# Performance work log

Hardware: AMD Instinct MI355X
Metric: run time of the kernel (lower is better)

Reference implementation:

```python
import jax, jax.numpy as jnp
import numpy as np

B_SZ, L, D_IN, D_MODEL, N_LAYERS, D_STATE, D_OUT = 32, 1024, 128, 256, 4, 64, 10
N2 = D_STATE // 2  # complex conjugate-pair modes


def setup_inputs() -> dict:
    key = jax.random.key(0)
    ks = jax.random.split(key, 12)
    H, N = D_MODEL, N2
    x = jax.random.normal(ks[0], (B_SZ, L, D_IN), jnp.float32)
    enc_w = jax.random.normal(ks[1], (D_IN, H), jnp.float32) / np.float32(np.sqrt(D_IN))
    enc_b = jnp.zeros((H,), jnp.float32)
    # S4D-diag params (diag-lin measure, real_type=exp): A = -exp(A_re_log) + i*A_im
    log_dt = jax.random.uniform(ks[2], (N_LAYERS, H), jnp.float32,
                                minval=np.float32(np.log(1e-3)), maxval=np.float32(np.log(1e-1)))
    A_re_log = jnp.full((N_LAYERS, H, N), np.float32(np.log(0.5)), jnp.float32)
    A_im = jnp.broadcast_to(np.float32(np.pi) * jnp.arange(N, dtype=jnp.float32),
                            (N_LAYERS, H, N)).copy()
    B_re = jnp.ones((N_LAYERS, H, N), jnp.float32)
    B_im = jnp.zeros((N_LAYERS, H, N), jnp.float32)
    C_re = jax.random.normal(ks[3], (N_LAYERS, H, N), jnp.float32) * np.float32(0.5 ** 0.5)
    C_im = jax.random.normal(ks[4], (N_LAYERS, H, N), jnp.float32) * np.float32(0.5 ** 0.5)
    D = jax.random.normal(ks[5], (N_LAYERS, H), jnp.float32)
    ln_w = jnp.ones((N_LAYERS, H), jnp.float32)
    ln_b = jnp.zeros((N_LAYERS, H), jnp.float32)
    out_w = jax.random.normal(ks[6], (N_LAYERS, H, 2 * H), jnp.float32) / np.float32(np.sqrt(H))
    out_b = jnp.zeros((N_LAYERS, 2 * H), jnp.float32)
    dec_w = jax.random.normal(ks[7], (H, D_OUT), jnp.float32) / np.float32(np.sqrt(H))
    dec_b = jnp.zeros((D_OUT,), jnp.float32)
    return dict(x=x, enc_w=enc_w, enc_b=enc_b, log_dt=log_dt, A_re_log=A_re_log, A_im=A_im,
                B_re=B_re, B_im=B_im, C_re=C_re, C_im=C_im, D=D, ln_w=ln_w, ln_b=ln_b,
                out_w=out_w, out_b=out_b, dec_w=dec_w, dec_b=dec_b)


def _layernorm(x, w, b):
    m = x.mean(-1, keepdims=True)
    v = ((x - m) ** 2).mean(-1, keepdims=True)
    return (x - m) * jax.lax.rsqrt(v + 1e-5) * w + b


def _s4_block(u, log_dt, A_re_log, A_im, B_re, B_im, C_re, C_im, Dp, out_w, out_b):
    # u: (B, L, H). Diagonal S4 (S4D) with ZOH discretization, FFT long-conv.
    H, N = A_re_log.shape
    Lq = u.shape[1]
    A = -jnp.exp(A_re_log) + 1j * A_im            # (H, N) complex, Re<0 stable
    dt = jnp.exp(log_dt)[:, None]                 # (H, 1)
    Bc = B_re + 1j * B_im
    Cc = C_re + 1j * C_im
    dtA = dt * A                                  # (H, N)
    dA = jnp.exp(dtA)
    dB = Bc * (dA - 1.0) / A                      # ZOH input matrix
    # Vandermonde kernel: K[h, l] = 2 * Re( sum_n C*dB * exp(dtA)^l )
    ell = jnp.arange(Lq, dtype=jnp.float32)
    P = jnp.exp(dtA[:, :, None] * ell)            # (H, N, L)
    K = 2.0 * jnp.einsum('hn,hnl->hl', Cc * dB, P).real  # (H, L) float32
    # causal conv via FFT at length 2L
    n_fft = 2 * Lq
    Kf = jnp.fft.rfft(K, n=n_fft, axis=-1)        # (H, L+1)
    Uf = jnp.fft.rfft(u, n=n_fft, axis=1)         # (B, L+1, H)
    y = jnp.fft.irfft(Uf * Kf.T[None], n=n_fft, axis=1)[:, :Lq]  # (B, L, H)
    y = y + u * Dp                                # skip connection D*u
    y = jax.nn.gelu(y)
    z = y @ out_w + out_b                         # position-wise output linear
    return z[..., :H] * jax.nn.sigmoid(z[..., H:])  # GLU


def reference(x, enc_w, enc_b, log_dt, A_re_log, A_im, B_re, B_im, C_re, C_im, D,
              ln_w, ln_b, out_w, out_b, dec_w, dec_b):
    h = x @ enc_w + enc_b                         # encoder: (B, L, d_model)
    for i in range(N_LAYERS):                     # postnorm residual stack
        z = _s4_block(h, log_dt[i], A_re_log[i], A_im[i], B_re[i], B_im[i],
                      C_re[i], C_im[i], D[i], out_w[i], out_b[i])
        h = z + h
        h = _layernorm(h, ln_w[i], ln_b[i])
    return h @ dec_w + dec_b                      # decoder: (B, L, d_output)
```

## Files before the change

### kernel.cpp

```cpp
#include <hip/hip_runtime.h>
#include <hip/hip_bf16.h>
#include <math.h>

#define B_SZ    32
#define LSEQ    1024
#define DIN     128
#define HDIM    256
#define NLAYERS 4
#define NSTATE  32
#define DOUT    10
#define M_ROWS  (B_SZ*LSEQ)
#define CH      64
#define NCH     (LSEQ/CH)
#define NBC     (B_SZ*NCH)

typedef __hip_bfloat16 bf16;
typedef __attribute__((ext_vector_type(8))) short bf16x8;
typedef __attribute__((ext_vector_type(4))) float f32x4;

__device__ __forceinline__ unsigned short f2bu(float x) {
    bf16 b = __float2bfloat16(x);
    return *(unsigned short*)&b;
}
__device__ __forceinline__ float bu2f(unsigned short u) {
    bf16 b = *(bf16*)&u;
    return __bfloat162float(b);
}

__device__ __forceinline__ float4 s4param(const float* __restrict__ log_dt,
                                          const float* __restrict__ A_re_log,
                                          const float* __restrict__ A_im,
                                          const float* __restrict__ B_re,
                                          const float* __restrict__ B_im,
                                          const float* __restrict__ C_re,
                                          const float* __restrict__ C_im,
                                          int layer, int h, int n) {
    int hn = layer * HDIM + h;
    int idx = hn * NSTATE + n;
    float dt   = expf(log_dt[hn]);
    float Are  = -expf(A_re_log[idx]);
    float Aim  = A_im[idx];
    float dtAre = dt * Are, dtAim = dt * Aim;
    float ea   = expf(dtAre);
    float dAre = ea * cosf(dtAim), dAim = ea * sinf(dtAim);
    float nre = dAre - 1.0f, nim = dAim;
    float inv = 1.0f / (Are * Are + Aim * Aim);
    float tre = (nre * Are + nim * Aim) * inv;
    float tim = (nim * Are - nre * Aim) * inv;
    float Brv = B_re[idx], Biv = B_im[idx];
    float dBre = Brv * tre - Biv * tim;
    float dBim = Brv * tim + Biv * tre;
    float Crv = C_re[idx], Civ = C_im[idx];
    float Wre = Crv * dBre - Civ * dBim;
    float Wim = Crv * dBim + Civ * dBre;
    return make_float4(dtAre, dtAim, Wre, Wim);
}

#define VMB_ (NLAYERS*HDIM*64*32/256)
#define TDB_ ((NLAYERS*HDIM*66+255)/256)
#define PAB_ (NLAYERS*NSTATE*HDIM/256)
#define WCB_ (NLAYERS*512*256/256)
__global__ void k_setup(const float* __restrict__ log_dt, const float* __restrict__ A_re_log,
                        const float* __restrict__ A_im, const float* __restrict__ B_re,
                        const float* __restrict__ B_im, const float* __restrict__ C_re,
                        const float* __restrict__ C_im, const float* __restrict__ out_w,
                        const float* __restrict__ enc_w, float* __restrict__ Td,
                        bf16* __restrict__ Vg, bf16* __restrict__ Mg,
                        float2* __restrict__ PA64, bf16* __restrict__ Wt,
                        bf16* __restrict__ Wet) {
    const float inv2pi = 0.15915494309189535f;
    const float twopi  = 6.283185307179586f;
    int bx = blockIdx.x;
    if (bx < VMB_) {
        int gid = bx * 256 + threadIdx.x;
        int jp = (gid & 31) * 2;
        int row = gid >> 5;
        int comp = row & 63, h = (row >> 6) & 255, layer = row >> 14;
        int n = comp >> 1, isIm = comp & 1;
        float4 q = s4param(log_dt, A_re_log, A_im, B_re, B_im, C_re, C_im, layer, h, n);
        unsigned int vpk = 0, mpk = 0;
#pragma unroll
        for (int e = 0; e < 2; ++e) {
            int j = jp + e;
            float dv = (float)(63 - j);
            float magv = __expf(dv * q.x);
            float pr = dv * q.y * inv2pi;
            float th = (pr - floorf(pr)) * twopi;
            float c = __cosf(th), s = __sinf(th);
            float vre = magv * (q.z * c - q.w * s);
            float vim = magv * (q.z * s + q.w * c);
            vpk |= (unsigned int)f2bu(isIm ? vim : vre) << (16 * e);
            float dm = (float)(j + 1);
            float magm = __expf(dm * q.x);
            float pr2 = dm * q.y * inv2pi;
            float th2 = (pr2 - floorf(pr2)) * twopi;
            float mv = isIm ? (-2.f * magm * __sinf(th2)) : (2.f * magm * __cosf(th2));
            mpk |= (unsigned int)f2bu(mv) << (16 * e);
        }
        {
            int mtv = comp >> 4, frv = comp & 15;
            int ksv = jp >> 5, qdv = (jp >> 3) & 3, ev = jp & 7;
            size_t voff = (size_t)(layer * 256 + h) * 4096
                        + ((size_t)((mtv * 2 + ksv) * 64) + qdv * 16 + frv) * 8 + ev;
            ((unsigned int*)Vg)[voff >> 1] = vpk;
        }
        ((unsigned int*)Mg)[(size_t)row * 32 + (jp >> 1)] = mpk;
    } else if (bx < VMB_ + TDB_) {
        int gid = (bx - VMB_) * 256 + threadIdx.x;
        int d = gid % 66;
        int lh = gid / 66;
        if (lh < NLAYERS * HDIM && d < 65) {
            int layer = lh >> 8, h = lh & 255;
            float fd = (float)d;
            float acc = 0.f;
            for (int n = 0; n < NSTATE; ++n) {
                float4 q = s4param(log_dt, A_re_log, A_im, B_re, B_im, C_re, C_im, layer, h, n);
                float mag = __expf(fd * q.x);
                float pr = fd * q.y * inv2pi;
                float th = (pr - floorf(pr)) * twopi;
                acc += mag * (q.z * __cosf(th) - q.w * __sinf(th));
            }
            Td[(size_t)lh * 66 + d] = 2.f * acc;
        }
    } else if (bx < VMB_ + TDB_ + PAB_) {
        int idx = (bx - VMB_ - TDB_) * 256 + threadIdx.x;
        int h = idx & 255, n = (idx >> 8) & 31, layer = idx >> 13;
        float4 q = s4param(log_dt, A_re_log, A_im, B_re, B_im, C_re, C_im, layer, h, n);
        float e64 = expf(64.0f * q.x);
        float ph  = 64.0f * q.y;
        PA64[idx] = make_float2(e64 * cosf(ph), e64 * sinf(ph));
    } else if (bx < VMB_ + TDB_ + PAB_ + WCB_) {
        int idx = (bx - VMB_ - TDB_ - PAB_) * 256 + threadIdx.x;
        int k = idx & 255;
        int n = (idx >> 8) & 511;
        int layer = idx >> 17;
        size_t off = (size_t)layer * (512 * 256)
                   + ((size_t)((n >> 4) * 8 + (k >> 5)) * 64 + (((k >> 3) & 3) * 16 + (n & 15))) * 8
                   + (k & 7);
        Wt[off] = __float2bfloat16(out_w[((size_t)(layer * 256 + k)) * 512 + n]);
    } else {
        int idx = (bx - VMB_ - TDB_ - PAB_ - WCB_) * 256 + threadIdx.x;
        int k = idx & 127, n = idx >> 7;
        Wet[idx] = __float2bfloat16(enc_w[(size_t)k * HDIM + n]);
    }
}

__global__ __launch_bounds__(256) void k_enc2(const float* __restrict__ X, const bf16* __restrict__ Wet,
                                              const float* __restrict__ bias, bf16* __restrict__ H,
                                              bf16* __restrict__ Ut) {
    __shared__ bf16 A_s[128 * 136];
    __shared__ bf16 B_s[64 * 136];
    int tid = threadIdx.x;
    int lane = tid & 63, wv = tid >> 6, quad = lane >> 4, fr = lane & 15;
    int m0 = blockIdx.x * 128, n0 = blockIdx.y * 64;
#pragma unroll
    for (int i = 0; i < 16; ++i) {
        int q = tid + i * 256, row = q >> 5, seg = q & 31;
        float4 v = *(const float4*)&X[(size_t)(m0 + row) * DIN + seg * 4];
        bf16* dst = &A_s[row * 136 + seg * 4];
        dst[0] = __float2bfloat16(v.x); dst[1] = __float2bfloat16(v.y);
        dst[2] = __float2bfloat16(v.z); dst[3] = __float2bfloat16(v.w);
    }
#pragma unroll
    for (int i = 0; i < 4; ++i) {
        int q = tid + i * 256, row = q >> 4, seg = q & 15;
        *(uint4*)&B_s[row * 136 + seg * 8] = *(const uint4*)&Wet[(size_t)(n0 + row) * DIN + seg * 8];
    }
    __syncthreads();
    f32x4 acc[2][4];
#pragma unroll
    for (int mt = 0; mt < 2; ++mt)
#pragma unroll
        for (int nt = 0; nt < 4; ++nt) acc[mt][nt] = (f32x4){0.f, 0.f, 0.f, 0.f};
#pragma unroll
    for (int ks = 0; ks < 4; ++ks) {
        bf16x8 a[2], b[4];
#pragma unroll
        for (int mt = 0; mt < 2; ++mt)
            a[mt] = *(const bf16x8*)&A_s[(wv * 32 + mt * 16 + fr) * 136 + ks * 32 + quad * 8];
#pragma unroll
        for (int nt = 0; nt < 4; ++nt)
            b[nt] = *(const bf16x8*)&B_s[(nt * 16 + fr) * 136 + ks * 32 + quad * 8];
#pragma unroll
        for (int mt = 0; mt < 2; ++mt)
#pragma unroll
            for (int nt = 0; nt < 4; ++nt)
                acc[mt][nt] = __builtin_amdgcn_mfma_f32_16x16x32_bf16(a[mt], b[nt], acc[mt][nt], 0, 0, 0);
    }
    __syncthreads();
#pragma unroll
    for (int mt = 0; mt < 2; ++mt)
#pragma unroll
        for (int nt = 0; nt < 4; ++nt) {
            int n = n0 + nt * 16 + fr;
            float bv = bias[n];
#pragma unroll
            for (int r = 0; r < 4; ++r) {
                int m = m0 + wv * 32 + mt * 16 + quad * 4 + r;
                float hv = acc[mt][nt][r] + bv;
                bf16 hb = __float2bfloat16(hv);
                H[(size_t)m * HDIM + n] = hb;
                B_s[(nt * 16 + fr) * 136 + (wv * 32 + mt * 16 + quad * 4 + r)] = hb;
            }
        }
    __syncthreads();
#pragma unroll
    for (int i = 0; i < 4; ++i) {
        int q = tid + i * 256, row = q >> 4, seg = q & 15;
        *(uint4*)&Ut[(size_t)(n0 + row) * M_ROWS + m0 + seg * 8] = *(uint4*)&B_s[row * 136 + seg * 8];
    }
}

__global__ __launch_bounds__(256) void k_conv(const bf16* __restrict__ Ut,
                                              const bf16* __restrict__ Vg,
                                              const bf16* __restrict__ Mg,
                                              const float* __restrict__ Tdl,
                                              const float2* __restrict__ PA,
                                              const float* __restrict__ Dw,
                                              bf16* __restrict__ Yt) {
    __shared__ bf16 A_s[64 * 136];
    __shared__ bf16 Eo_s[128 * 72];
    int h = blockIdx.x, bc0 = blockIdx.y * 128;
    int tid = threadIdx.x;
    int lane = tid & 63, wv = tid >> 6, quad = lane >> 4, fr = lane & 15;
    const float* Tdh = Tdl + (size_t)h * 66;
    const bf16* Uh = Ut + (size_t)h * M_ROWS + (size_t)bc0 * 64;
    bf16x8 va[2][4], ub[2][2];
#pragma unroll
    for (int ks = 0; ks < 2; ++ks) {
#pragma unroll
        for (int mt = 0; mt < 4; ++mt)
            va[ks][mt] = *(const bf16x8*)&Vg[(size_t)h * 4096 + ((size_t)((mt * 2 + ks) * 64) + lane) * 8];
#pragma unroll
        for (int nf = 0; nf < 2; ++nf)
            ub[ks][nf] = *(const bf16x8*)&Uh[(size_t)(wv * 32 + nf * 16 + fr) * 64 + ks * 32 + quad * 8];
    }
#pragma unroll
    for (int i = 0; i < 2; ++i) {
        int q = tid + i * 256, comp = q >> 3, seg = q & 7;
        uint4 v = *(const uint4*)&Mg[((size_t)h * 64 + comp) * 64 + seg * 8];
        const bf16* pv = (const bf16*)&v;
#pragma unroll
        for (int e = 0; e < 8; ++e) A_s[(seg * 8 + e) * 136 + 64 + comp] = pv[e];
    }
#pragma unroll
    for (int i = 0; i < 16; ++i) {
        int q = tid + i * 256, l = q >> 6, j = q & 63, d = l - j;
        A_s[l * 136 + j] = __float2bfloat16(d >= 0 ? Tdh[d] : 0.f);
    }
    f32x4 eacc[4][2];
#pragma unroll
    for (int mt = 0; mt < 4; ++mt)
#pragma unroll
        for (int nf = 0; nf < 2; ++nf) eacc[mt][nf] = (f32x4){0.f, 0.f, 0.f, 0.f};
#pragma unroll
    for (int ks = 0; ks < 2; ++ks)
#pragma unroll
        for (int mt = 0; mt < 4; ++mt)
#pragma unroll
            for (int nf = 0; nf < 2; ++nf)
                eacc[mt][nf] = __builtin_amdgcn_mfma_f32_16x16x32_bf16(va[ks][mt], ub[ks][nf], eacc[mt][nf], 0, 0, 0);
#pragma unroll
    for (int mt = 0; mt < 4; ++mt)
#pragma unroll
        for (int nf = 0; nf < 2; ++nf) {
            int bc = wv * 32 + nf * 16 + fr;
#pragma unroll
            for (int r = 0; r < 4; r += 2) {
                int comp = mt * 16 + quad * 4 + r;
                *(unsigned int*)&Eo_s[bc * 72 + comp] =
                    (unsigned int)f2bu(eacc[mt][nf][r]) | ((unsigned int)f2bu(eacc[mt][nf][r + 1]) << 16);
            }
        }
    __syncthreads();
    {
        int bl = tid >> 5, n = tid & 31;
        float2 a = PA[n * HDIM + h];
        float cr = 0.f, ci = 0.f;
#pragma unroll
        for (int c = 0; c < NCH; ++c) {
            int bc = bl * NCH + c;
            unsigned int* slot = (unsigned int*)&Eo_s[bc * 72 + 2 * n];
            unsigned int ev = *slot;
            *slot = (unsigned int)f2bu(cr) | ((unsigned int)f2bu(ci) << 16);
            float er = bu2f((unsigned short)(ev & 0xffff));
            float ei = bu2f((unsigned short)(ev >> 16));
            float nr = fmaf(a.x, cr, fmaf(-a.y, ci, er));
            ci = fmaf(a.x, ci, fmaf(a.y, cr, ei));
            cr = nr;
        }
    }
    __syncthreads();
    f32x4 acc[4][2];
#pragma unroll
    for (int mt = 0; mt < 4; ++mt)
#pragma unroll
        for (int nf = 0; nf < 2; ++nf) acc[mt][nf] = (f32x4){0.f, 0.f, 0.f, 0.f};
#pragma unroll
    for (int ks = 0; ks < 4; ++ks) {
        bf16x8 a[4], b[2];
#pragma unroll
        for (int mt = 0; mt < 4; ++mt)
            a[mt] = *(const bf16x8*)&A_s[(mt * 16 + fr) * 136 + ks * 32 + quad * 8];
#pragma unroll
        for (int nf = 0; nf < 2; ++nf) {
            int row = wv * 32 + nf * 16 + fr;
            b[nf] = (ks < 2) ? ub[ks][nf]
                             : *(const bf16x8*)&Eo_s[row * 72 + (ks - 2) * 32 + quad * 8];
        }
#pragma unroll
        for (int mt = 0; mt < 4; ++mt)
#pragma unroll
            for (int nf = 0; nf < 2; ++nf)
                acc[mt][nf] = __builtin_amdgcn_mfma_f32_16x16x32_bf16(a[mt], b[nf], acc[mt][nf], 0, 0, 0);
    }
    float Dv = Dw[h];
#pragma unroll
    for (int mt = 0; mt < 4; ++mt)
#pragma unroll
        for (int nf = 0; nf < 2; ++nf) {
            int bcl = wv * 32 + nf * 16 + fr;
            uint2 uv = *(const uint2*)&Uh[(size_t)bcl * 64 + mt * 16 + quad * 4];
            const bf16* up = (const bf16*)&uv;
#pragma unroll
            for (int r = 0; r < 4; ++r) {
                int l = mt * 16 + quad * 4 + r;
                float u = __bfloat162float(up[r]);
                float v = fmaf(Dv, u, acc[mt][nf][r]);
                float z2 = 1.5957691216057308f * (v + 0.044715f * v * v * v);
                Eo_s[bcl * 72 + l] = __float2bfloat16(v / (1.f + __expf(-z2)));
            }
        }
    __syncthreads();
#pragma unroll
    for (int i = 0; i < 4; ++i) {
        int q = tid + i * 256, row = q >> 3, c8 = q & 7;
        *(uint4*)&Yt[(size_t)h * M_ROWS + (size_t)(bc0 + row) * 64 + c8 * 8] =
            *(uint4*)&Eo_s[row * 72 + c8 * 8];
    }
}

__global__ __launch_bounds__(256) void k_gluln(const bf16* __restrict__ Yt,
                                               const bf16* __restrict__ Wt,
                                               const float* __restrict__ wb,
                                               bf16* __restrict__ Hb,
                                               const float* __restrict__ w,
                                               const float* __restrict__ bbias,
                                               bf16* __restrict__ Ut,
                                               const float* __restrict__ dw,
                                               const float* __restrict__ db,
                                               float* __restrict__ outp, int mode) {
    __shared__ __align__(16) bf16 A_s[32 * 264];
    __shared__ __align__(16) bf16 t_s2[256 * 40];
    __shared__ float red[2][8][32];
    __shared__ float stat[2][32];
    __shared__ float w_s[256], b_s[256];
    __shared__ float ob_s[512];
    __shared__ float db_s[16];
    int tid = threadIdx.x;
    int lane = tid & 63, wv = tid >> 6;
    int quad = lane >> 4, fr = lane & 15;
    int m0 = blockIdx.x * 32;
    w_s[tid] = w[tid]; b_s[tid] = bbias[tid];
    ob_s[tid] = wb[tid]; ob_s[256 + tid] = wb[256 + tid];
    if (mode == 1 && tid < DOUT) db_s[tid] = db[tid];
    {
        int mg = tid & 7, hg = tid >> 3;
        uint2 rowv[8];
#pragma unroll
        for (int e = 0; e < 8; ++e)
            rowv[e] = *(const uint2*)&Yt[(size_t)(hg * 8 + e) * M_ROWS + m0 + mg * 4];
#pragma unroll
        for (int j = 0; j < 4; ++j) {
            unsigned int pk[4];
#pragma unroll
            for (int k2 = 0; k2 < 4; ++k2) {
                unsigned int lo = ((const unsigned short*)&rowv[2 * k2])[j];
                unsigned int hi = ((const unsigned short*)&rowv[2 * k2 + 1])[j];
                pk[k2] = lo | (hi << 16);
            }
            *(uint4*)&A_s[(mg * 4 + j) * 264 + hg * 8] = *(uint4*)pk;
        }
    }
    f32x4 acc1[2][4], acc2[2][4];
#pragma unroll
    for (int mt = 0; mt < 2; ++mt)
#pragma unroll
        for (int nt = 0; nt < 4; ++nt) {
            acc1[mt][nt] = (f32x4){0.f, 0.f, 0.f, 0.f};
            acc2[mt][nt] = (f32x4){0.f, 0.f, 0.f, 0.f};
        }
    __syncthreads();

#define LOAD_B(d1, d2, KS) do { \
    _Pragma("unroll") \
    for (int nt = 0; nt < 4; ++nt) { \
        d1[nt] = *(const bf16x8*)&Wt[((size_t)((wv * 4 + nt) * 8 + (KS)) * 64 + lane) * 8]; \
        d2[nt] = *(const bf16x8*)&Wt[((size_t)((16 + wv * 4 + nt) * 8 + (KS)) * 64 + lane) * 8]; \
    } } while (0)

#define DO_MFMA(bb1, bb2, KS) do { \
    bf16x8 afr[2]; \
    _Pragma("unroll") \
    for (int mt = 0; mt < 2; ++mt) \
        afr[mt] = *(const bf16x8*)&A_s[(mt * 16 + fr) * 264 + (KS) * 32 + quad * 8]; \
    _Pragma("unroll") \
    for (int mt = 0; mt < 2; ++mt) \
        _Pragma("unroll") \
        for (int nt = 0; nt < 4; ++nt) { \
            acc1[mt][nt] = __builtin_amdgcn_mfma_f32_16x16x32_bf16(afr[mt], bb1[nt], acc1[mt][nt], 0, 0, 0); \
            acc2[mt][nt] = __builtin_amdgcn_mfma_f32_16x16x32_bf16(afr[mt], bb2[nt], acc2[mt][nt], 0, 0, 0); \
        } } while (0)

    {
        bf16x8 p1[4], p2[4], q1[4], q2[4];
        LOAD_B(p1, p2, 0);
#pragma unroll
        for (int kp = 0; kp < 4; ++kp) {
            LOAD_B(q1, q2, 2 * kp + 1);
            DO_MFMA(p1, p2, 2 * kp);
            if (kp < 3) LOAD_B(p1, p2, 2 * kp + 2);
            DO_MFMA(q1, q2, 2 * kp + 1);
        }
    }
#undef LOAD_B
#undef DO_MFMA

    __syncthreads();
#pragma unroll
    for (int mt = 0; mt < 2; ++mt)
#pragma unroll
        for (int nt = 0; nt < 4; ++nt) {
            int n = wv * 64 + nt * 16 + fr;
            float b1v = ob_s[n], b2v = ob_s[HDIM + n];
#pragma unroll
            for (int r = 0; r < 4; ++r) {
                int m = mt * 16 + quad * 4 + r;
                float z1 = acc1[mt][nt][r] + b1v;
                float z2 = acc2[mt][nt][r] + b2v;
                A_s[m * 264 + n] = __float2bfloat16(z1 / (1.0f + __expf(-z2)));
            }
        }
    __syncthreads();
    int rr = tid & 31, qd = tid >> 5;
    const bf16* Hr = Hb + (size_t)(m0 + rr) * HDIM + qd * 32;
    float rv[32];
    float sum = 0.f, sq = 0.f;
#pragma unroll
    for (int j = 0; j < 32; j += 8) {
        uint4 gv = *(uint4*)&A_s[rr * 264 + qd * 32 + j];
        uint4 hv4 = *(const uint4*)&Hr[j];
        const bf16* gp = (const bf16*)&gv;
        const bf16* hp = (const bf16*)&hv4;
#pragma unroll
        for (int e = 0; e < 8; ++e) {
            float v = __bfloat162float(gp[e]) + __bfloat162float(hp[e]);
            rv[j + e] = v; sum += v; sq += v * v;
        }
    }
    red[0][qd][rr] = sum; red[1][qd][rr] = sq;
    __syncthreads();
    if (tid < 32) {
        float s = 0.f, s2 = 0.f;
#pragma unroll
        for (int q = 0; q < 8; ++q) { s += red[0][q][tid]; s2 += red[1][q][tid]; }
        float mean = s * (1.f / HDIM);
        float var = s2 * (1.f / HDIM) - mean * mean;
        stat[0][tid] = mean; stat[1][tid] = rsqrtf(var + 1e-5f);
    }
    __syncthreads();
    float mean = stat[0][rr], rstd = stat[1][rr];
#pragma unroll
    for (int j = 0; j < 32; ++j)
        rv[j] = (rv[j] - mean) * rstd * w_s[qd * 32 + j] + b_s[qd * 32 + j];
    if (mode == 0) {
        bf16* Hw = Hb + (size_t)(m0 + rr) * HDIM + qd * 32;
#pragma unroll
        for (int j = 0; j < 32; j += 8) {
            unsigned int pk[4];
#pragma unroll
            for (int e = 0; e < 4; ++e)
                pk[e] = (unsigned int)f2bu(rv[j + 2 * e]) | ((unsigned int)f2bu(rv[j + 2 * e + 1]) << 16);
            *(uint4*)&Hw[j] = *(uint4*)pk;
        }
    }
#pragma unroll
    for (int j = 0; j < 32; ++j)
        t_s2[(qd * 32 + j) * 40 + rr] = __float2bfloat16(rv[j]);
    if (mode == 1) {
        float* dwf = (float*)A_s;
        for (int e = tid; e < HDIM * DOUT; e += 256) dwf[e] = dw[e];
    }
    __syncthreads();
    if (mode == 0) {
#pragma unroll
        for (int i = 0; i < 4; ++i) {
            int q = tid + i * 256, row = q >> 2, seg = q & 3;
            *(uint4*)&Ut[(size_t)row * M_ROWS + m0 + seg * 8] = *(uint4*)&t_s2[row * 40 + seg * 8];
        }
    } else {
        const float* dwf = (const float*)A_s;
        for (int q = tid; q < 32 * DOUT; q += 256) {
            int ml = q / DOUT, o = q - ml * DOUT;
            float acc = db_s[o];
#pragma unroll 8
            for (int hh = 0; hh < HDIM; ++hh)
                acc = fmaf(__bfloat162float(t_s2[hh * 40 + ml]), dwf[hh * DOUT + o], acc);
            outp[(size_t)(m0 + ml) * DOUT + o] = acc;
        }
    }
}

extern "C" void kernel_launch(void* const* d_in, const int* in_sizes, int n_in,
                              void* d_out, int out_size, void* d_ws, size_t ws_size,
                              hipStream_t stream) {
    const float* x        = (const float*)d_in[0];
    const float* enc_w    = (const float*)d_in[1];
    const float* enc_b    = (const float*)d_in[2];
    const float* log_dt   = (const float*)d_in[3];
    const float* A_re_log = (const float*)d_in[4];
    const float* A_im     = (const float*)d_in[5];
    const float* B_re     = (const float*)d_in[6];
    const float* B_im     = (const float*)d_in[7];
    const float* C_re     = (const float*)d_in[8];
    const float* C_im     = (const float*)d_in[9];
    const float* Dp       = (const float*)d_in[10];
    const float* ln_w     = (const float*)d_in[11];
    const float* ln_b     = (const float*)d_in[12];
    const float* out_w    = (const float*)d_in[13];
    const float* out_b    = (const float*)d_in[14];
    const float* dec_w    = (const float*)d_in[15];
    const float* dec_b    = (const float*)d_in[16];
    float* outp = (float*)d_out;

    float* w = (float*)d_ws;
    const size_t PWE = (size_t)NLAYERS * NSTATE * HDIM;
    const size_t MH  = (size_t)M_ROWS * HDIM;
    const size_t VME = (size_t)NLAYERS * HDIM * 64 * 64;
    float2* PA64 = (float2*)(w + 4 * PWE);
    float*  Td   = w + 6 * PWE;
    bf16*   Hbuf = (bf16*)(Td + (size_t)NLAYERS * HDIM * 66);
    bf16*   Ut   = Hbuf + MH;
    bf16*   Yt   = Ut + MH;
    bf16*   Wt   = Yt + MH;
    bf16*   Wet  = Wt + (size_t)NLAYERS * 512 * HDIM;
    bf16*   Vg   = Wet + (size_t)HDIM * DIN;
    bf16*   Mg   = Vg + VME;

    {
        int total = VMB_ + TDB_ + PAB_ + WCB_ + HDIM * DIN / 256;
        k_setup<<<total, 256, 0, stream>>>(log_dt, A_re_log, A_im, B_re, B_im, C_re, C_im,
                                           out_w, enc_w, Td, Vg, Mg, PA64, Wt, Wet);
    }

    dim3 ge(M_ROWS / 128, HDIM / 64);
    k_enc2<<<ge, 256, 0, stream>>>(x, Wet, enc_b, Hbuf, Ut);

    dim3 gconv(HDIM, NBC / 128);
    for (int layer = 0; layer < NLAYERS; ++layer) {
        const float2* pal = PA64 + (size_t)layer * NSTATE * HDIM;
        const float*  tdl = Td + (size_t)layer * HDIM * 66;
        const bf16*   vgl = Vg + (size_t)layer * HDIM * 64 * 64;
        const bf16*   mgl = Mg + (size_t)layer * HDIM * 64 * 64;
        k_conv<<<gconv, 256, 0, stream>>>(Ut, vgl, mgl, tdl, pal, Dp + layer * HDIM, Yt);
        k_gluln<<<M_ROWS / 32, 256, 0, stream>>>(Yt, Wt + (size_t)layer * 512 * HDIM,
                                                 out_b + layer * 2 * HDIM, Hbuf,
                                                 ln_w + layer * HDIM, ln_b + layer * HDIM,
                                                 Ut, dec_w, dec_b, outp,
                                                 layer == NLAYERS - 1 ? 1 : 0);
    }
}
```

Before: 334.6 us.

## Drop transpose staging buffer in GLU+LN kernel, write Ut directly and reduce decoder in registers

Removes the t_s2 shared-memory transpose tile and the ob_s bias buffer, which lowers LDS use per block. The GLU bias now comes from registers, and the transposed Ut is written straight from registers with per-element strided 2-byte global stores. The decoder instead computes per-thread partial dot products from register values and reduces them across the 8 column groups via shared memory. The aim is higher occupancy and fewer barriers, at the risk of less coalesced (though contiguous across the warp) Ut stores.

```diff
diff --git a/kernel.cpp b/kernel.cpp
--- a/kernel.cpp
+++ b/kernel.cpp
@@ -351,19 +351,22 @@
                                                const float* __restrict__ db,
                                                float* __restrict__ outp, int mode) {
     __shared__ __align__(16) bf16 A_s[32 * 264];
-    __shared__ __align__(16) bf16 t_s2[256 * 40];
     __shared__ float red[2][8][32];
     __shared__ float stat[2][32];
     __shared__ float w_s[256], b_s[256];
-    __shared__ float ob_s[512];
     __shared__ float db_s[16];
     int tid = threadIdx.x;
     int lane = tid & 63, wv = tid >> 6;
     int quad = lane >> 4, fr = lane & 15;
     int m0 = blockIdx.x * 32;
     w_s[tid] = w[tid]; b_s[tid] = bbias[tid];
-    ob_s[tid] = wb[tid]; ob_s[256 + tid] = wb[256 + tid];
     if (mode == 1 && tid < DOUT) db_s[tid] = db[tid];
+    float bias1[4], bias2[4];
+#pragma unroll
+    for (int nt = 0; nt < 4; ++nt) {
+        bias1[nt] = wb[wv * 64 + nt * 16 + fr];
+        bias2[nt] = wb[HDIM + wv * 64 + nt * 16 + fr];
+    }
     {
         int mg = tid & 7, hg = tid >> 3;
         uint2 rowv[8];
@@ -432,12 +435,11 @@
 #pragma unroll
         for (int nt = 0; nt < 4; ++nt) {
             int n = wv * 64 + nt * 16 + fr;
-            float b1v = ob_s[n], b2v = ob_s[HDIM + n];
 #pragma unroll
             for (int r = 0; r < 4; ++r) {
                 int m = mt * 16 + quad * 4 + r;
-                float z1 = acc1[mt][nt][r] + b1v;
-                float z2 = acc2[mt][nt][r] + b2v;
+                float z1 = acc1[mt][nt][r] + bias1[nt];
+                float z2 = acc2[mt][nt][r] + bias2[nt];
                 A_s[m * 264 + n] = __float2bfloat16(z1 / (1.0f + __expf(-z2)));
             }
         }
@@ -483,30 +485,38 @@
                 pk[e] = (unsigned int)f2bu(rv[j + 2 * e]) | ((unsigned int)f2bu(rv[j + 2 * e + 1]) << 16);
             *(uint4*)&Hw[j] = *(uint4*)pk;
         }
-    }
-#pragma unroll
-    for (int j = 0; j < 32; ++j)
-        t_s2[(qd * 32 + j) * 40 + rr] = __float2bfloat16(rv[j]);
-    if (mode == 1) {
+        bf16* Up = Ut + (size_t)(qd * 32) * M_ROWS + m0 + rr;
+#pragma unroll
+        for (int j = 0; j < 32; ++j)
+            Up[(size_t)j * M_ROWS] = __float2bfloat16(rv[j]);
+    } else {
         float* dwf = (float*)A_s;
         for (int e = tid; e < HDIM * DOUT; e += 256) dwf[e] = dw[e];
-    }
-    __syncthreads();
-    if (mode == 0) {
-#pragma unroll
-        for (int i = 0; i < 4; ++i) {
-            int q = tid + i * 256, row = q >> 2, seg = q & 3;
-            *(uint4*)&Ut[(size_t)row * M_ROWS + m0 + seg * 8] = *(uint4*)&t_s2[row * 40 + seg * 8];
-        }
-    } else {
-        const float* dwf = (const float*)A_s;
-        for (int q = tid; q < 32 * DOUT; q += 256) {
-            int ml = q / DOUT, o = q - ml * DOUT;
-            float acc = db_s[o];
-#pragma unroll 8
-            for (int hh = 0; hh < HDIM; ++hh)
-                acc = fmaf(__bfloat162float(t_s2[hh * 40 + ml]), dwf[hh * DOUT + o], acc);
-            outp[(size_t)(m0 + ml) * DOUT + o] = acc;
+        __syncthreads();
+        float part[DOUT];
+#pragma unroll
+        for (int o = 0; o < DOUT; ++o) part[o] = 0.f;
+#pragma unroll
+        for (int j = 0; j < 32; ++j) {
+            float tv = rv[j];
+            const float* dr = &dwf[(qd * 32 + j) * DOUT];
+#pragma unroll
+            for (int o = 0; o < DOUT; ++o) part[o] = fmaf(tv, dr[o], part[o]);
+        }
+#pragma unroll
+        for (int oc = 0; oc < 5; ++oc) {
+            red[0][qd][rr] = part[2 * oc];
+            red[1][qd][rr] = part[2 * oc + 1];
+            __syncthreads();
+            if (tid < 64) {
+                int rl = tid & 31, ph = tid >> 5;
+                float s = 0.f;
+#pragma unroll
+                for (int q = 0; q < 8; ++q) s += red[ph][q][rl];
+                int o = 2 * oc + ph;
+                outp[(size_t)(m0 + rl) * DOUT + o] = s + db_s[o];
+            }
+            __syncthreads();
         }
     }
 }
```

Result: faster. 323.5 us (-3.3%).

## Process two 32-row tiles per GLU-LN block with double-buffered staging

Applied to the files above, without the earlier changes.

Each k_gluln block now handles 64 rows as two 32-row tiles, double-buffering the A tile in shared memory so the second tile's Yt and residual loads and packing overlap the first tile's GEMM and layernorm. Bias values move into registers, and the transposed Ut write goes straight from registers with strided per-element stores instead of a shared-memory transpose. The final decoder projection becomes a per-thread partial product followed by a shared-memory reduction. The cost is half as many blocks, more registers per thread, and less coalesced Ut stores.

```diff
diff --git a/kernel.cpp b/kernel.cpp
--- a/kernel.cpp
+++ b/kernel.cpp
@@ -350,47 +350,43 @@
                                                const float* __restrict__ dw,
                                                const float* __restrict__ db,
                                                float* __restrict__ outp, int mode) {
-    __shared__ __align__(16) bf16 A_s[32 * 264];
-    __shared__ __align__(16) bf16 t_s2[256 * 40];
+    __shared__ __align__(16) bf16 A_s[2][32 * 264];
     __shared__ float red[2][8][32];
     __shared__ float stat[2][32];
     __shared__ float w_s[256], b_s[256];
-    __shared__ float ob_s[512];
     __shared__ float db_s[16];
     int tid = threadIdx.x;
     int lane = tid & 63, wv = tid >> 6;
     int quad = lane >> 4, fr = lane & 15;
-    int m0 = blockIdx.x * 32;
+    int mg = tid & 7, hg = tid >> 3;
+    int rr = tid & 31, qd = tid >> 5;
+    int mbase = blockIdx.x * 64;
     w_s[tid] = w[tid]; b_s[tid] = bbias[tid];
-    ob_s[tid] = wb[tid]; ob_s[256 + tid] = wb[256 + tid];
     if (mode == 1 && tid < DOUT) db_s[tid] = db[tid];
-    {
-        int mg = tid & 7, hg = tid >> 3;
-        uint2 rowv[8];
-#pragma unroll
-        for (int e = 0; e < 8; ++e)
-            rowv[e] = *(const uint2*)&Yt[(size_t)(hg * 8 + e) * M_ROWS + m0 + mg * 4];
-#pragma unroll
-        for (int j = 0; j < 4; ++j) {
-            unsigned int pk[4];
-#pragma unroll
-            for (int k2 = 0; k2 < 4; ++k2) {
-                unsigned int lo = ((const unsigned short*)&rowv[2 * k2])[j];
-                unsigned int hi = ((const unsigned short*)&rowv[2 * k2 + 1])[j];
-                pk[k2] = lo | (hi << 16);
-            }
-            *(uint4*)&A_s[(mg * 4 + j) * 264 + hg * 8] = *(uint4*)pk;
-        }
-    }
+    float bias1[4], bias2[4];
+#pragma unroll
+    for (int nt = 0; nt < 4; ++nt) {
+        bias1[nt] = wb[wv * 64 + nt * 16 + fr];
+        bias2[nt] = wb[HDIM + wv * 64 + nt * 16 + fr];
+    }
+    uint2 rowv[8];
+    uint4 hbv0[4], hbv1[4];
     f32x4 acc1[2][4], acc2[2][4];
-#pragma unroll
-    for (int mt = 0; mt < 2; ++mt)
-#pragma unroll
-        for (int nt = 0; nt < 4; ++nt) {
-            acc1[mt][nt] = (f32x4){0.f, 0.f, 0.f, 0.f};
-            acc2[mt][nt] = (f32x4){0.f, 0.f, 0.f, 0.f};
-        }
-    __syncthreads();
+    float rv[32];
+    float sum, sq;
+
+#define PACK_A(BUF) do { \
+    _Pragma("unroll") \
+    for (int j = 0; j < 4; ++j) { \
+        unsigned int pk[4]; \
+        _Pragma("unroll") \
+        for (int k2 = 0; k2 < 4; ++k2) { \
+            unsigned int lo = ((const unsigned short*)&rowv[2 * k2])[j]; \
+            unsigned int hi = ((const unsigned short*)&rowv[2 * k2 + 1])[j]; \
+            pk[k2] = lo | (hi << 16); \
+        } \
+        *(uint4*)&A_s[BUF][(mg * 4 + j) * 264 + hg * 8] = *(uint4*)pk; \
+    } } while (0)
 
 #define LOAD_B(d1, d2, KS) do { \
     _Pragma("unroll") \
@@ -399,11 +395,11 @@
         d2[nt] = *(const bf16x8*)&Wt[((size_t)((16 + wv * 4 + nt) * 8 + (KS)) * 64 + lane) * 8]; \
     } } while (0)
 
-#define DO_MFMA(bb1, bb2, KS) do { \
+#define DO_MFMA(bb1, bb2, KS, BUF) do { \
     bf16x8 afr[2]; \
     _Pragma("unroll") \
     for (int mt = 0; mt < 2; ++mt) \
-        afr[mt] = *(const bf16x8*)&A_s[(mt * 16 + fr) * 264 + (KS) * 32 + quad * 8]; \
+        afr[mt] = *(const bf16x8*)&A_s[BUF][(mt * 16 + fr) * 264 + (KS) * 32 + quad * 8]; \
     _Pragma("unroll") \
     for (int mt = 0; mt < 2; ++mt) \
         _Pragma("unroll") \
@@ -412,103 +408,147 @@
             acc2[mt][nt] = __builtin_amdgcn_mfma_f32_16x16x32_bf16(afr[mt], bb2[nt], acc2[mt][nt], 0, 0, 0); \
         } } while (0)
 
-    {
-        bf16x8 p1[4], p2[4], q1[4], q2[4];
-        LOAD_B(p1, p2, 0);
-#pragma unroll
-        for (int kp = 0; kp < 4; ++kp) {
-            LOAD_B(q1, q2, 2 * kp + 1);
-            DO_MFMA(p1, p2, 2 * kp);
-            if (kp < 3) LOAD_B(p1, p2, 2 * kp + 2);
-            DO_MFMA(q1, q2, 2 * kp + 1);
-        }
-    }
+#define RUN_GEMM(BUF) do { \
+    _Pragma("unroll") \
+    for (int mt = 0; mt < 2; ++mt) \
+        _Pragma("unroll") \
+        for (int nt = 0; nt < 4; ++nt) { \
+            acc1[mt][nt] = (f32x4){0.f, 0.f, 0.f, 0.f}; \
+            acc2[mt][nt] = (f32x4){0.f, 0.f, 0.f, 0.f}; \
+        } \
+    bf16x8 p1[4], p2[4], q1[4], q2[4]; \
+    LOAD_B(p1, p2, 0); \
+    _Pragma("unroll") \
+    for (int kp = 0; kp < 4; ++kp) { \
+        LOAD_B(q1, q2, 2 * kp + 1); \
+        DO_MFMA(p1, p2, 2 * kp, BUF); \
+        if (kp < 3) LOAD_B(p1, p2, 2 * kp + 2); \
+        DO_MFMA(q1, q2, 2 * kp + 1, BUF); \
+    } } while (0)
+
+#define GLU_WRITE(BUF) do { \
+    _Pragma("unroll") \
+    for (int mt = 0; mt < 2; ++mt) \
+        _Pragma("unroll") \
+        for (int nt = 0; nt < 4; ++nt) { \
+            int n = wv * 64 + nt * 16 + fr; \
+            _Pragma("unroll") \
+            for (int r = 0; r < 4; ++r) { \
+                int m = mt * 16 + quad * 4 + r; \
+                float z1 = acc1[mt][nt][r] + bias1[nt]; \
+                float z2 = acc2[mt][nt][r] + bias2[nt]; \
+                A_s[BUF][m * 264 + n] = __float2bfloat16(z1 / (1.0f + __expf(-z2))); \
+            } \
+        } } while (0)
+
+#define LN_PHASE(BUF, HBV, M0) do { \
+    sum = 0.f; sq = 0.f; \
+    _Pragma("unroll") \
+    for (int i4 = 0; i4 < 4; ++i4) { \
+        uint4 gv = *(uint4*)&A_s[BUF][rr * 264 + qd * 32 + i4 * 8]; \
+        const bf16* gp = (const bf16*)&gv; \
+        const bf16* hp = (const bf16*)&HBV[i4]; \
+        _Pragma("unroll") \
+        for (int e = 0; e < 8; ++e) { \
+            float v = __bfloat162float(gp[e]) + __bfloat162float(hp[e]); \
+            rv[i4 * 8 + e] = v; sum += v; sq += v * v; \
+        } \
+    } \
+    red[0][qd][rr] = sum; red[1][qd][rr] = sq; \
+    __syncthreads(); \
+    if (tid < 32) { \
+        float s = 0.f, s2 = 0.f; \
+        _Pragma("unroll") \
+        for (int q = 0; q < 8; ++q) { s += red[0][q][tid]; s2 += red[1][q][tid]; } \
+        float mean_ = s * (1.f / HDIM); \
+        float var_ = s2 * (1.f / HDIM) - mean_ * mean_; \
+        stat[0][tid] = mean_; stat[1][tid] = rsqrtf(var_ + 1e-5f); \
+    } \
+    __syncthreads(); \
+    { \
+        float mean = stat[0][rr], rstd = stat[1][rr]; \
+        _Pragma("unroll") \
+        for (int j = 0; j < 32; ++j) \
+            rv[j] = (rv[j] - mean) * rstd * w_s[qd * 32 + j] + b_s[qd * 32 + j]; \
+    } \
+    if (mode == 0) { \
+        bf16* Hw = Hb + (size_t)((M0) + rr) * HDIM + qd * 32; \
+        _Pragma("unroll") \
+        for (int j = 0; j < 32; j += 8) { \
+            unsigned int pk[4]; \
+            _Pragma("unroll") \
+            for (int e = 0; e < 4; ++e) \
+                pk[e] = (unsigned int)f2bu(rv[j + 2 * e]) | ((unsigned int)f2bu(rv[j + 2 * e + 1]) << 16); \
+            *(uint4*)&Hw[j] = *(uint4*)pk; \
+        } \
+        bf16* Up = Ut + (size_t)(qd * 32) * M_ROWS + (M0) + rr; \
+        _Pragma("unroll") \
+        for (int j = 0; j < 32; ++j) \
+            Up[(size_t)j * M_ROWS] = __float2bfloat16(rv[j]); \
+    } else { \
+        __syncthreads(); \
+        float* dwf = (float*)A_s[BUF]; \
+        for (int e = tid; e < HDIM * DOUT; e += 256) dwf[e] = dw[e]; \
+        __syncthreads(); \
+        float part[DOUT]; \
+        _Pragma("unroll") \
+        for (int o = 0; o < DOUT; ++o) part[o] = 0.f; \
+        _Pragma("unroll") \
+        for (int j = 0; j < 32; ++j) { \
+            float tv = rv[j]; \
+            const float* dr = &dwf[(qd * 32 + j) * DOUT]; \
+            _Pragma("unroll") \
+            for (int o = 0; o < DOUT; ++o) part[o] = fmaf(tv, dr[o], part[o]); \
+        } \
+        _Pragma("unroll") \
+        for (int oc = 0; oc < 5; ++oc) { \
+            red[0][qd][rr] = part[2 * oc]; \
+            red[1][qd][rr] = part[2 * oc + 1]; \
+            __syncthreads(); \
+            if (tid < 64) { \
+                int rl = tid & 31, ph = tid >> 5; \
+                float s = 0.f; \
+                _Pragma("unroll") \
+                for (int q = 0; q < 8; ++q) s += red[ph][q][rl]; \
+                int o = 2 * oc + ph; \
+                outp[(size_t)((M0) + rl) * DOUT + o] = s + db_s[o]; \
+            } \
+            __syncthreads(); \
+        } \
+    } } while (0)
+
+#pragma unroll
+    for (int e = 0; e < 8; ++e)
+        rowv[e] = *(const uint2*)&Yt[(size_t)(hg * 8 + e) * M_ROWS + mbase + mg * 4];
+#pragma unroll
+    for (int i = 0; i < 4; ++i)
+        hbv0[i] = *(const uint4*)&Hb[(size_t)(mbase + rr) * HDIM + qd * 32 + i * 8];
+    PACK_A(0);
+    __syncthreads();
+#pragma unroll
+    for (int e = 0; e < 8; ++e)
+        rowv[e] = *(const uint2*)&Yt[(size_t)(hg * 8 + e) * M_ROWS + mbase + 32 + mg * 4];
+#pragma unroll
+    for (int i = 0; i < 4; ++i)
+        hbv1[i] = *(const uint4*)&Hb[(size_t)(mbase + 32 + rr) * HDIM + qd * 32 + i * 8];
+    RUN_GEMM(0);
+    __syncthreads();
+    GLU_WRITE(0);
+    PACK_A(1);
+    __syncthreads();
+    LN_PHASE(0, hbv0, mbase);
+    RUN_GEMM(1);
+    __syncthreads();
+    GLU_WRITE(1);
+    __syncthreads();
+    LN_PHASE(1, hbv1, mbase + 32);
+
+#undef PACK_A
 #undef LOAD_B
 #undef DO_MFMA
-
-    __syncthreads();
-#pragma unroll
-    for (int mt = 0; mt < 2; ++mt)
-#pragma unroll
-        for (int nt = 0; nt < 4; ++nt) {
-            int n = wv * 64 + nt * 16 + fr;
-            float b1v = ob_s[n], b2v = ob_s[HDIM + n];
-#pragma unroll
-            for (int r = 0; r < 4; ++r) {
-                int m = mt * 16 + quad * 4 + r;
-                float z1 = acc1[mt][nt][r] + b1v;
-                float z2 = acc2[mt][nt][r] + b2v;
-                A_s[m * 264 + n] = __float2bfloat16(z1 / (1.0f + __expf(-z2)));
-            }
-        }
-    __syncthreads();
-    int rr = tid & 31, qd = tid >> 5;
-    const bf16* Hr = Hb + (size_t)(m0 + rr) * HDIM + qd * 32;
-    float rv[32];
-    float sum = 0.f, sq = 0.f;
-#pragma unroll
-    for (int j = 0; j < 32; j += 8) {
-        uint4 gv = *(uint4*)&A_s[rr * 264 + qd * 32 + j];
-        uint4 hv4 = *(const uint4*)&Hr[j];
-        const bf16* gp = (const bf16*)&gv;
-        const bf16* hp = (const bf16*)&hv4;
-#pragma unroll
-        for (int e = 0; e < 8; ++e) {
-            float v = __bfloat162float(gp[e]) + __bfloat162float(hp[e]);
-            rv[j + e] = v; sum += v; sq += v * v;
-        }
-    }
-    red[0][qd][rr] = sum; red[1][qd][rr] = sq;
-    __syncthreads();
-    if (tid < 32) {
-        float s = 0.f, s2 = 0.f;
-#pragma unroll
-        for (int q = 0; q < 8; ++q) { s += red[0][q][tid]; s2 += red[1][q][tid]; }
-        float mean = s * (1.f / HDIM);
-        float var = s2 * (1.f / HDIM) - mean * mean;
-        stat[0][tid] = mean; stat[1][tid] = rsqrtf(var + 1e-5f);
-    }
-    __syncthreads();
-    float mean = stat[0][rr], rstd = stat[1][rr];
-#pragma unroll
-    for (int j = 0; j < 32; ++j)
-        rv[j] = (rv[j] - mean) * rstd * w_s[qd * 32 + j] + b_s[qd * 32 + j];
-    if (mode == 0) {
-        bf16* Hw = Hb + (size_t)(m0 + rr) * HDIM + qd * 32;
-#pragma unroll
-        for (int j = 0; j < 32; j += 8) {
-            unsigned int pk[4];
-#pragma unroll
-            for (int e = 0; e < 4; ++e)
-                pk[e] = (unsigned int)f2bu(rv[j + 2 * e]) | ((unsigned int)f2bu(rv[j + 2 * e + 1]) << 16);
-            *(uint4*)&Hw[j] = *(uint4*)pk;
-        }
-    }
-#pragma unroll
-    for (int j = 0; j < 32; ++j)
-        t_s2[(qd * 32 + j) * 40 + rr] = __float2bfloat16(rv[j]);
-    if (mode == 1) {
-        float* dwf = (float*)A_s;
-        for (int e = tid; e < HDIM * DOUT; e += 256) dwf[e] = dw[e];
-    }
-    __syncthreads();
-    if (mode == 0) {
-#pragma unroll
-        for (int i = 0; i < 4; ++i) {
-            int q = tid + i * 256, row = q >> 2, seg = q & 3;
-            *(uint4*)&Ut[(size_t)row * M_ROWS + m0 + seg * 8] = *(uint4*)&t_s2[row * 40 + seg * 8];
-        }
-    } else {
-        const float* dwf = (const float*)A_s;
-        for (int q = tid; q < 32 * DOUT; q += 256) {
-            int ml = q / DOUT, o = q - ml * DOUT;
-            float acc = db_s[o];
-#pragma unroll 8
-            for (int hh = 0; hh < HDIM; ++hh)
-                acc = fmaf(__bfloat162float(t_s2[hh * 40 + ml]), dwf[hh * DOUT + o], acc);
-            outp[(size_t)(m0 + ml) * DOUT + o] = acc;
-        }
-    }
+#undef RUN_GEMM
+#undef GLU_WRITE
+#undef LN_PHASE
 }
 
 extern "C" void kernel_launch(void* const* d_in, const int* in_sizes, int n_in,
@@ -563,7 +603,7 @@
         const bf16*   vgl = Vg + (size_t)layer * HDIM * 64 * 64;
         const bf16*   mgl = Mg + (size_t)layer * HDIM * 64 * 64;
         k_conv<<<gconv, 256, 0, stream>>>(Ut, vgl, mgl, tdl, pal, Dp + layer * HDIM, Yt);
-        k_gluln<<<M_ROWS / 32, 256, 0, stream>>>(Yt, Wt + (size_t)layer * 512 * HDIM,
+        k_gluln<<<M_ROWS / 64, 256, 0, stream>>>(Yt, Wt + (size_t)layer * 512 * HDIM,
                                                  out_b + layer * 2 * HDIM, Hbuf,
                                                  ln_w + layer * HDIM, ln_b + layer * HDIM,
                                                  Ut, dec_w, dec_b, outp,
```

Result: slower. 352.0 us (+5.2%).
